# Performance work log

Measured on AMD Instinct MI355X. Metric: run time of the kernel, lower is better.

## Reference

```python
import jax, jax.numpy as jnp
import numpy as np

C = 32
C_Z = 128
S = 256   # MSA depth
N = 384   # residues


def setup_inputs() -> dict:
    key = jax.random.key(0)
    ks = jax.random.split(key, 7)
    m = jax.random.normal(ks[0], (S, N, C), dtype=jnp.float32)
    gamma = jnp.ones((C,), dtype=jnp.float32)
    beta = jnp.zeros((C,), dtype=jnp.float32)
    # projections stored as [in, out]
    W1 = jax.random.normal(ks[1], (C, C), dtype=jnp.float32) / np.sqrt(C)
    W2 = jax.random.normal(ks[2], (C, C), dtype=jnp.float32) / np.sqrt(C)
    W3 = jax.random.normal(ks[3], (C * C, C_Z), dtype=jnp.float32) / np.sqrt(C * C)
    b3 = jnp.zeros((C_Z,), dtype=jnp.float32)
    return {"m": m, "gamma": gamma, "beta": beta, "W1": W1, "W2": W2, "W3": W3, "b3": b3}


def reference(m, gamma, beta, W1, W2, W3, b3):
    # LayerNorm over channel dim
    mu = jnp.mean(m, axis=-1, keepdims=True)
    var = jnp.mean(jnp.square(m - mu), axis=-1, keepdims=True)
    mn = (m - mu) * jax.lax.rsqrt(var + 1e-5) * gamma + beta
    a = jnp.einsum('sic,cd->sid', mn, W1)  # [s, n, c]
    b = jnp.einsum('sic,cd->sid', mn, W2)  # [s, n, c]
    # outer product, mean over MSA dim s -> [n, n, c, c]
    o = jnp.einsum('sic,sjd->ijcd', a, b) / a.shape[0]
    o = o.reshape(o.shape[0], o.shape[1], C * C)  # [n, n, c*c]
    z = o @ W3 + b3  # [n, n, c_z]
    return z
```

## Files before the change

kernel.cpp:

```cpp
#include <hip/hip_runtime.h>

#define S_DEPTH 256
#define NRES 384
#define CIN 32
#define CZ 128
#define MDIM (NRES * CIN)

typedef short bf16x8 __attribute__((ext_vector_type(8)));
typedef short short4v __attribute__((ext_vector_type(4)));
typedef float f32x4 __attribute__((ext_vector_type(4)));

static __device__ __forceinline__ unsigned short f2bf(float f) {
  unsigned int u = __float_as_uint(f);
  unsigned int r = (u + 0x7fffu + ((u >> 16) & 1u)) >> 16;
  return (unsigned short)r;
}

static __device__ __forceinline__ void gld16(const void* g, void* l) {
  __builtin_amdgcn_global_load_lds((__attribute__((address_space(1))) void*)(g),
                                   (__attribute__((address_space(3))) void*)(l),
                                   16, 0, 0);
}

__global__ __launch_bounds__(256) void k_pre(
    const float* __restrict__ mm, const float* __restrict__ gamma,
    const float* __restrict__ beta, const float* __restrict__ W1,
    const float* __restrict__ W2, const float* __restrict__ W3,
    unsigned short* __restrict__ aT, unsigned short* __restrict__ bT,
    unsigned short* __restrict__ W3T) {
  __shared__ __align__(16) char sraw[256 * 33 * 4];
  __shared__ __align__(16) char mn_raw[256 * 80];
  const int t = threadIdx.x;

  if (blockIdx.x < 16) {
    unsigned short (*tile)[72] = (unsigned short(*)[72])sraw;
    const int b = blockIdx.x;
    const int d0 = (b & 7) * 4;
    const int e0 = (b >> 3) * 64;
#pragma unroll
    for (int iter = 0; iter < 32; ++iter) {
      int lr_ = iter * 4 + (t >> 6);
      int c = lr_ >> 2, dl = lr_ & 3;
      int q = c * 32 + d0 + dl;
      tile[lr_][t & 63] = f2bf(W3[q * 128 + e0 + (t & 63)]);
    }
    __syncthreads();
    const int e_l = t >> 2;
    const int dl = t & 3;
    unsigned short* dst = W3T + (((size_t)(d0 + dl) * 128) + e0 + e_l) * 32;
#pragma unroll
    for (int j = 0; j < 32; ++j) dst[j] = tile[j * 4 + dl][e_l];
    return;
  }

  float* buf = (float*)sraw;
  const int i = blockIdx.x - 16;

#pragma unroll
  for (int it = 0; it < 8; ++it) {
    int s = it * 32 + (t >> 3);
    int c4 = (t & 7) * 4;
    const float4 v = *(const float4*)(mm + ((size_t)s * NRES + i) * CIN + c4);
    buf[s * 33 + c4 + 0] = v.x;
    buf[s * 33 + c4 + 1] = v.y;
    buf[s * 33 + c4 + 2] = v.z;
    buf[s * 33 + c4 + 3] = v.w;
  }
  __syncthreads();

  {
    float x[32];
#pragma unroll
    for (int k = 0; k < 32; ++k) x[k] = buf[t * 33 + k];
    float mu = 0.f;
#pragma unroll
    for (int k = 0; k < 32; ++k) mu += x[k];
    mu *= (1.f / 32.f);
    float var = 0.f;
#pragma unroll
    for (int k = 0; k < 32; ++k) {
      float dk = x[k] - mu;
      var += dk * dk;
    }
    var *= (1.f / 32.f);
    float inv = rsqrtf(var + 1e-5f);
    char* row = mn_raw + t * 80;
#pragma unroll
    for (int q = 0; q < 4; ++q) {
      bf16x8 pk;
#pragma unroll
      for (int j = 0; j < 8; ++j) {
        int k = q * 8 + j;
        pk[j] = (short)f2bf((x[k] - mu) * inv * gamma[k] + beta[k]);
      }
      *(bf16x8*)(row + q * 16) = pk;
    }
  }

  const int l = t & 63;
  const int w = t >> 6;
  const int lr = l & 15;
  const int quad = l >> 4;

  bf16x8 wfr[4];
#pragma unroll
  for (int nf = 0; nf < 4; ++nf) {
    const float* W = (nf < 2) ? W1 : W2;
    const int c = lr + (nf & 1) * 16;
#pragma unroll
    for (int j = 0; j < 8; ++j)
      wfr[nf][j] = (short)f2bf(W[(quad * 8 + j) * 32 + c]);
  }

  __syncthreads();

  f32x4 acc2[4][4];
#pragma unroll
  for (int sg = 0; sg < 4; ++sg) {
    const bf16x8 mfrag =
        *(const bf16x8*)(mn_raw + (size_t)(w * 64 + sg * 16 + lr) * 80 + quad * 16);
#pragma unroll
    for (int nf = 0; nf < 4; ++nf) {
      f32x4 z = {0.f, 0.f, 0.f, 0.f};
      acc2[sg][nf] = __builtin_amdgcn_mfma_f32_16x16x32_bf16(wfr[nf], mfrag, z, 0, 0, 0);
    }
  }

  const size_t rowbase = (size_t)w * MDIM + (size_t)i * 32;
#pragma unroll
  for (int sg = 0; sg < 4; ++sg)
#pragma unroll
    for (int nf = 0; nf < 4; ++nf) {
      unsigned short* tgt = (nf < 2) ? aT : bT;
      const int c0 = (nf & 1) * 16 + quad * 4;
      const int s = sg * 16 + lr;
#pragma unroll
      for (int r = 0; r < 4; ++r)
        tgt[(rowbase + c0 + r) * 64 + s] = f2bf(acc2[sg][nf][r]);
    }
}

__global__ __launch_bounds__(512, 2) void k_opm(
    const unsigned short* __restrict__ aT, const unsigned short* __restrict__ bT,
    const unsigned short* __restrict__ W3T, const float* __restrict__ b3,
    float* __restrict__ out) {
  __shared__ __align__(16) char smem[131072];
  const int t = threadIdx.x;
  const int w = t >> 6;
  const int l = t & 63;
  const int lr = l & 15;
  const int quad = l >> 4;
  const int wm = w >> 2, wn = w & 3;

  const int g = blockIdx.x;
  const int xcd = g & 7;
  const int rr = g >> 3;
  const int bx = rr / 6;
  const int by = xcd * 6 + (rr - bx * 6);
  const int m0 = by * 256;
  const int n0 = bx * 256;

  f32x4 acc[8][4];
#pragma unroll
  for (int mt = 0; mt < 8; ++mt)
#pragma unroll
    for (int nt = 0; nt < 4; ++nt) {
      acc[mt][nt][0] = 0.f; acc[mt][nt][1] = 0.f;
      acc[mt][nt][2] = 0.f; acc[mt][nt][3] = 0.f;
    }

  const int laneoff = (l >> 3) * 64 + (((l & 7) ^ (l >> 3)) * 8);
  const int r8 = lr & 7;

  {
    const unsigned short* aS = aT + (size_t)m0 * 64;
    const unsigned short* bS = bT + (size_t)n0 * 64;
#pragma unroll
    for (int p_ = 0; p_ < 4; ++p_) {
      int ch = p_ * 8 + w;
      gld16(aS + ch * 512 + laneoff, smem + ch * 1024);
      gld16(bS + ch * 512 + laneoff, smem + 32768 + ch * 1024);
    }
  }
  __syncthreads();

  for (int kt = 0; kt < 4; ++kt) {
    if (kt < 3) {
      char* nb = smem + ((kt + 1) & 1) * 65536;
      const unsigned short* aS = aT + ((size_t)(kt + 1) * MDIM + m0) * 64;
      const unsigned short* bS = bT + ((size_t)(kt + 1) * MDIM + n0) * 64;
#pragma unroll
      for (int p_ = 0; p_ < 4; ++p_) {
        int ch = p_ * 8 + w;
        gld16(aS + ch * 512 + laneoff, nb + ch * 1024);
        gld16(bS + ch * 512 + laneoff, nb + 32768 + ch * 1024);
      }
    }
    const char* cb = smem + (kt & 1) * 65536;
    const char* cbB = cb + 32768;

#pragma unroll
    for (int ks = 0; ks < 2; ++ks) {
      const int segoff = (((ks * 4 + quad) ^ r8) << 4);
      bf16x8 af[8];
#pragma unroll
      for (int mt = 0; mt < 8; ++mt) {
        int chunk = wm * 16 + mt * 2 + (lr >> 3);
        af[mt] = *(const bf16x8*)(cb + chunk * 1024 + r8 * 128 + segoff);
      }
#pragma unroll
      for (int nt = 0; nt < 4; ++nt) {
        int chunk = wn * 8 + nt * 2 + (lr >> 3);
        bf16x8 bfr = *(const bf16x8*)(cbB + chunk * 1024 + r8 * 128 + segoff);
#pragma unroll
        for (int mt = 0; mt < 8; ++mt)
          acc[mt][nt] =
              __builtin_amdgcn_mfma_f32_16x16x32_bf16(af[mt], bfr, acc[mt][nt], 0, 0, 0);
      }
    }
    __syncthreads();
  }

  const float scale = 1.0f / 256.0f;
#pragma unroll
  for (int mt = 0; mt < 8; ++mt) {
    int i_l = wm * 4 + (mt >> 1);
    int chc = 2 * (mt & 1) + (quad >> 1);
#pragma unroll
    for (int nt = 0; nt < 4; ++nt) {
      int j_l = wn * 2 + (nt >> 1);
      int d = (nt & 1) * 16 + lr;
      int p = i_l * 8 + j_l;
      int ch = d * 4 + chc;
      int key = (p ^ d) & 7;
      int off = p * 2048 + ((ch ^ key) << 4) + 8 * (quad & 1);
      short4v pk;
      pk[0] = (short)f2bf(acc[mt][nt][0] * scale);
      pk[1] = (short)f2bf(acc[mt][nt][1] * scale);
      pk[2] = (short)f2bf(acc[mt][nt][2] * scale);
      pk[3] = (short)f2bf(acc[mt][nt][3] * scale);
      *(short4v*)(smem + off) = pk;
    }
  }
  __syncthreads();

  f32x4 zacc[4];
#pragma unroll
  for (int a = 0; a < 4; ++a) {
    zacc[a][0] = 0.f; zacc[a][1] = 0.f; zacc[a][2] = 0.f; zacc[a][3] = 0.f;
  }
  const float bias = b3[w * 16 + lr];

  const unsigned short* wg = W3T + (size_t)(w * 16 + lr) * 32 + quad * 8;

  bf16x8 wcur = *(const bf16x8*)(wg);
#pragma unroll
  for (int kq = 0; kq < 32; ++kq) {
    bf16x8 wnxt;
    if (kq < 31) wnxt = *(const bf16x8*)(wg + (size_t)(kq + 1) * 4096);
    bf16x8 aef[4];
#pragma unroll
    for (int mte = 0; mte < 4; ++mte) {
      int row = mte * 16 + lr;
      int ch = kq * 4 + quad;
      int key = (row ^ kq) & 7;
      aef[mte] = *(const bf16x8*)(smem + row * 2048 + ((ch ^ key) << 4));
    }
#pragma unroll
    for (int mte = 0; mte < 4; ++mte)
      zacc[mte] = __builtin_amdgcn_mfma_f32_16x16x32_bf16(aef[mte], wcur, zacc[mte], 0, 0, 0);
    wcur = wnxt;
  }

  const int i0 = by * 8, j0 = bx * 8;
  const int e = w * 16 + lr;
#pragma unroll
  for (int mte = 0; mte < 4; ++mte)
#pragma unroll
    for (int r = 0; r < 4; ++r) {
      int p = mte * 16 + quad * 4 + r;
      out[(((size_t)(i0 + (p >> 3))) * NRES + (j0 + (p & 7))) * CZ + e] =
          zacc[mte][r] + bias;
    }
}

extern "C" void kernel_launch(void* const* d_in, const int* in_sizes, int n_in,
                              void* d_out, int out_size, void* d_ws, size_t ws_size,
                              hipStream_t stream) {
  const float* m = (const float*)d_in[0];
  const float* gamma = (const float*)d_in[1];
  const float* beta = (const float*)d_in[2];
  const float* W1 = (const float*)d_in[3];
  const float* W2 = (const float*)d_in[4];
  const float* W3 = (const float*)d_in[5];
  const float* b3 = (const float*)d_in[6];
  float* out = (float*)d_out;

  unsigned short* aT = (unsigned short*)d_ws;
  unsigned short* bT = aT + (size_t)MDIM * S_DEPTH;
  unsigned short* W3T = bT + (size_t)MDIM * S_DEPTH;

  k_pre<<<400, 256, 0, stream>>>(m, gamma, beta, W1, W2, W3, aT, bT, W3T);
  k_pre<<<400, 256, 0, stream>>>(m, gamma, beta, W1, W2, W3, aT, bT, W3T);
  k_opm<<<2304, 512, 0, stream>>>(aT, bT, W3T, b3, out);
}
```

Measured before the change: 218.7 us.

## Retile W3 projection per-wave as 2x2 MFMA block and drop duplicate pre-pass launch

Each of the 8 waves previously computed 64 pair-rows by 16 output channels, reading all 4 A-fragments from LDS per k-step. Now each wave handles 32 rows by 32 channels, loading two W3 fragments and two LDS A-fragments per step, which cuts LDS reads per MFMA. The second, redundant k_pre launch is also removed, eliminating a whole duplicate preprocessing kernel. The retiling doubles global W3 loads per wave and changes the output store pattern.

```diff
diff --git a/kernel.cpp b/kernel.cpp
--- a/kernel.cpp
+++ b/kernel.cpp
@@ -244,43 +244,58 @@
   }
   __syncthreads();
 
-  f32x4 zacc[4];
-#pragma unroll
-  for (int a = 0; a < 4; ++a) {
-    zacc[a][0] = 0.f; zacc[a][1] = 0.f; zacc[a][2] = 0.f; zacc[a][3] = 0.f;
-  }
-  const float bias = b3[w * 16 + lr];
-
-  const unsigned short* wg = W3T + (size_t)(w * 16 + lr) * 32 + quad * 8;
-
-  bf16x8 wcur = *(const bf16x8*)(wg);
+  const int pb = w >> 2;
+  const int eb = w & 3;
+  f32x4 zacc[2][2];
+#pragma unroll
+  for (int a = 0; a < 2; ++a)
+#pragma unroll
+    for (int e_ = 0; e_ < 2; ++e_) {
+      zacc[a][e_][0] = 0.f; zacc[a][e_][1] = 0.f;
+      zacc[a][e_][2] = 0.f; zacc[a][e_][3] = 0.f;
+    }
+  const float bias0 = b3[eb * 32 + lr];
+  const float bias1 = b3[eb * 32 + 16 + lr];
+
+  const unsigned short* wg0 = W3T + (size_t)(eb * 32 + lr) * 32 + quad * 8;
+  const unsigned short* wg1 = wg0 + 512;
+
+  bf16x8 wc0 = *(const bf16x8*)(wg0);
+  bf16x8 wc1 = *(const bf16x8*)(wg1);
 #pragma unroll
   for (int kq = 0; kq < 32; ++kq) {
-    bf16x8 wnxt;
-    if (kq < 31) wnxt = *(const bf16x8*)(wg + (size_t)(kq + 1) * 4096);
-    bf16x8 aef[4];
-#pragma unroll
-    for (int mte = 0; mte < 4; ++mte) {
-      int row = mte * 16 + lr;
+    bf16x8 wn0, wn1;
+    if (kq < 31) {
+      wn0 = *(const bf16x8*)(wg0 + (size_t)(kq + 1) * 4096);
+      wn1 = *(const bf16x8*)(wg1 + (size_t)(kq + 1) * 4096);
+    }
+    bf16x8 aef[2];
+#pragma unroll
+    for (int mte = 0; mte < 2; ++mte) {
+      int row_ = pb * 32 + mte * 16 + lr;
       int ch = kq * 4 + quad;
-      int key = (row ^ kq) & 7;
-      aef[mte] = *(const bf16x8*)(smem + row * 2048 + ((ch ^ key) << 4));
-    }
-#pragma unroll
-    for (int mte = 0; mte < 4; ++mte)
-      zacc[mte] = __builtin_amdgcn_mfma_f32_16x16x32_bf16(aef[mte], wcur, zacc[mte], 0, 0, 0);
-    wcur = wnxt;
+      int key = (row_ ^ kq) & 7;
+      aef[mte] = *(const bf16x8*)(smem + row_ * 2048 + ((ch ^ key) << 4));
+    }
+#pragma unroll
+    for (int mte = 0; mte < 2; ++mte) {
+      zacc[mte][0] =
+          __builtin_amdgcn_mfma_f32_16x16x32_bf16(aef[mte], wc0, zacc[mte][0], 0, 0, 0);
+      zacc[mte][1] =
+          __builtin_amdgcn_mfma_f32_16x16x32_bf16(aef[mte], wc1, zacc[mte][1], 0, 0, 0);
+    }
+    wc0 = wn0; wc1 = wn1;
   }
 
   const int i0 = by * 8, j0 = bx * 8;
-  const int e = w * 16 + lr;
-#pragma unroll
-  for (int mte = 0; mte < 4; ++mte)
+#pragma unroll
+  for (int mte = 0; mte < 2; ++mte)
 #pragma unroll
     for (int r = 0; r < 4; ++r) {
-      int p = mte * 16 + quad * 4 + r;
-      out[(((size_t)(i0 + (p >> 3))) * NRES + (j0 + (p & 7))) * CZ + e] =
-          zacc[mte][r] + bias;
+      int p = pb * 32 + mte * 16 + quad * 4 + r;
+      size_t base = (((size_t)(i0 + (p >> 3))) * NRES + (j0 + (p & 7))) * CZ;
+      out[base + eb * 32 + lr] = zacc[mte][0][r] + bias0;
+      out[base + eb * 32 + 16 + lr] = zacc[mte][1][r] + bias1;
     }
 }
 
@@ -301,6 +316,5 @@
   unsigned short* W3T = bT + (size_t)MDIM * S_DEPTH;
 
   k_pre<<<400, 256, 0, stream>>>(m, gamma, beta, W1, W2, W3, aT, bT, W3T);
-  k_pre<<<400, 256, 0, stream>>>(m, gamma, beta, W1, W2, W3, aT, bT, W3T);
   k_opm<<<2304, 512, 0, stream>>>(aT, bT, W3T, b3, out);
 }
```

Result: slower. 237.1 us (+8.4%).
